# Kernel tuning notes

Hardware: AMD Instinct MI355X
Metric: run time of the kernel (lower is better)

## Reference

```python
import jax, jax.numpy as jnp
import numpy as np

DIM = 96
NHEAD = 8
HEAD_DIM = DIM // NHEAD  # 12
N, L, S = 1, 262144, 262144  # 64^3 flattened 3D volume tokens
EPS_LA = 1e-6
EPS_LN = 1e-5


def layer_norm(x, w, b):
    mu = jnp.mean(x, axis=-1, keepdims=True)
    var = jnp.mean((x - mu) ** 2, axis=-1, keepdims=True)
    return (x - mu) * jax.lax.rsqrt(var + EPS_LN) * w + b


def setup_inputs() -> dict:
    key = jax.random.key(0)
    ks = jax.random.split(key, 24)
    std = 0.02
    def w(k, shape):
        return jax.random.normal(k, shape, dtype=jnp.float32) * std
    inp = {
        "mr_seg_feat_flatten": jax.random.normal(ks[0], (N, L, DIM), dtype=jnp.float32),
        "ct2mr_attention_flatten": jax.random.normal(ks[1], (N, L, DIM), dtype=jnp.float32),
        "warp_ctfeat": jax.random.normal(ks[2], (N, S, DIM), dtype=jnp.float32),
        # CrossmodalSemanticsCalibration params (torch Linear weights: [out, in])
        "w_qkv": w(ks[3], (DIM, DIM)),
        "w_qkv2": w(ks[4], (DIM, DIM)),
        "ln1_w": jnp.ones((DIM,), jnp.float32),
        "ln1_b": jnp.zeros((DIM,), jnp.float32),
        "ln2_w": jnp.ones((2 * DIM,), jnp.float32),
        "ln2_b": jnp.zeros((2 * DIM,), jnp.float32),
        "mlp_fc1_w": w(ks[5], (2 * DIM, 2 * DIM)),
        "mlp_fc1_b": jnp.zeros((2 * DIM,), jnp.float32),
        "mlp_fc2_w": w(ks[6], (DIM, 2 * DIM)),
        "mlp_fc2_b": jnp.zeros((DIM,), jnp.float32),
        # StructureAttention(96, 8) params
        "sa_wq": w(ks[7], (DIM, DIM)),
        "sa_wk": w(ks[8], (DIM, DIM)),
        "sa_wv": w(ks[9], (DIM, DIM)),
        "sa_merge": w(ks[10], (DIM, DIM)),
        "sa_mlp_w1": w(ks[11], (2 * DIM, 2 * DIM)),
        "sa_mlp_w2": w(ks[12], (DIM, 2 * DIM)),
        "sa_ln1_w": jnp.ones((DIM,), jnp.float32),
        "sa_ln1_b": jnp.zeros((DIM,), jnp.float32),
        "sa_ln2_w": jnp.ones((DIM,), jnp.float32),
        "sa_ln2_b": jnp.zeros((DIM,), jnp.float32),
    }
    return inp


def _forward(mr_seg_feat_flatten, ct2mr_attention_flatten, warp_ctfeat,
             w_qkv, w_qkv2, ln1_w, ln1_b, ln2_w, ln2_b,
             mlp_fc1_w, mlp_fc1_b, mlp_fc2_w, mlp_fc2_b,
             sa_wq, sa_wk, sa_wv, sa_merge, sa_mlp_w1, sa_mlp_w2,
             sa_ln1_w, sa_ln1_b, sa_ln2_w, sa_ln2_b):
    # CrossmodalSemanticsCalibration.forward (ct2mr_attention_flatten is unused, as in torch)
    x0 = layer_norm(mr_seg_feat_flatten, ln1_w, ln1_b)
    shortcut = x0 @ w_qkv.T                        # [N, L, C]
    y = shortcut @ w_qkv2.T                        # [N, L, C]

    # StructureAttention(y, warp_ctfeat) with kernelized LinearAttention
    n, l, c = y.shape
    s = warp_ctfeat.shape[1]
    q = (y @ sa_wq.T).reshape(n, l, NHEAD, HEAD_DIM)
    k = (warp_ctfeat @ sa_wk.T).reshape(n, s, NHEAD, HEAD_DIM)
    v = (warp_ctfeat @ sa_wv.T).reshape(n, s, NHEAD, HEAD_DIM)
    Q = jax.nn.elu(q) + 1.0
    K = jax.nn.elu(k) + 1.0
    KV = jnp.einsum('nshd,nshv->nhdv', K, v / s)   # [N, H, d, d]
    Z = 1.0 / (jnp.einsum('nlhd,nhd->nlh', Q, K.sum(axis=1)) + EPS_LA)
    msg = jnp.einsum('nlhd,nhdv,nlh->nlhv', Q, KV, Z) * s
    msg = msg.reshape(n, l, c) @ sa_merge.T
    msg = layer_norm(msg, sa_ln1_w, sa_ln1_b)
    h = jnp.concatenate([y, msg], axis=-1) @ sa_mlp_w1.T
    h = jax.nn.relu(h) @ sa_mlp_w2.T
    h = layer_norm(h, sa_ln2_w, sa_ln2_b)
    x = y + h                                      # StructureAttention output

    # fuse with shortcut, final Mlp (GELU, exact erf as torch default)
    x = jnp.concatenate([x, shortcut], axis=-1)    # [N, L, 2C]
    x = layer_norm(x, ln2_w, ln2_b)
    x = jax.nn.gelu(x @ mlp_fc1_w.T + mlp_fc1_b, approximate=False)
    x = x @ mlp_fc2_w.T + mlp_fc2_b
    return x                                       # [N, L, C]


def reference(mr_seg_feat_flatten, ct2mr_attention_flatten, warp_ctfeat,
              w_qkv, w_qkv2, ln1_w, ln1_b, ln2_w, ln2_b,
              mlp_fc1_w, mlp_fc1_b, mlp_fc2_w, mlp_fc2_b,
              sa_wq, sa_wk, sa_wv, sa_merge, sa_mlp_w1, sa_mlp_w2,
              sa_ln1_w, sa_ln1_b, sa_ln2_w, sa_ln2_b):
    return _forward(mr_seg_feat_flatten, ct2mr_attention_flatten, warp_ctfeat,
                    w_qkv, w_qkv2, ln1_w, ln1_b, ln2_w, ln2_b,
                    mlp_fc1_w, mlp_fc1_b, mlp_fc2_w, mlp_fc2_b,
                    sa_wq, sa_wk, sa_wv, sa_merge, sa_mlp_w1, sa_mlp_w2,
                    sa_ln1_w, sa_ln1_b, sa_ln2_w, sa_ln2_b)
```

## Files before the change

### kernel.cpp

```cpp
#include <hip/hip_runtime.h>
#include <hip/hip_bf16.h>


typedef __attribute__((ext_vector_type(8))) short short8;
typedef __attribute__((ext_vector_type(4))) float f32x4;
typedef __attribute__((ext_vector_type(4))) unsigned int uint4v;

#define WS_FLAG 0
#define WS_PKV  512
#define WS_PSV  (WS_PKV + 16*9216*4)
#define WS_PSE  (WS_PSV + 16*96*4)
#define WS_KSUM (WS_PSE + 16*96*4)
#define WS_KSTOT (WS_KSUM + 96*4)
#define WS_CM   (WS_KSTOT + 64)
#define WS_BDT  (WS_CM + 768*4)
#define WS_WB   (WS_BDT + 9216*2)
#define WS_VEC  (WS_WB + 165888*2)

#define OQKV   0
#define OQKV2  9216
#define OWQ    18432
#define OWK    27648
#define OWV    36864
#define OMERGE 46080
#define OW1    55296
#define OW2    92160
#define OFC1   110592
#define OFC2   147456
#define VLN1W 0
#define VLN1B 96
#define VLN2W 192
#define VLN2B 384
#define VFC1B 576
#define VFC2B 768
#define VSA1W 864
#define VSA1B 960
#define VSA2W 1056
#define VSA2B 1152

struct InPtrs { const void* p[23]; };

__device__ inline float b2f(unsigned short x) {
  union { unsigned u; float f; } c; c.u = ((unsigned)x) << 16; return c.f;
}
__device__ inline unsigned short f2b(float f) {
  __hip_bfloat16 h = __float2bfloat16(f);
  return *(unsigned short*)&h;
}
__device__ inline uint2 pack4bf(float v0, float v1, float v2, float v3) {
  uint2 r;
  r.x = (unsigned)f2b(v0) | ((unsigned)f2b(v1) << 16);
  r.y = (unsigned)f2b(v2) | ((unsigned)f2b(v3) << 16);
  return r;
}

__global__ void probe_k(const void* in0, unsigned* flag) {
  int tid = threadIdx.x;
  const unsigned short* u = (const unsigned short*)in0;
  int cnt = 0;
  for (int j = 0; j < 8; ++j) {
    unsigned short v = u[(tid * 8 + j) * 2];
    unsigned e = (v >> 7) & 0xFF;
    if ((e >= 110 && e <= 141) || ((v & 0x7FFF) == 0)) cnt++;
  }
  for (int o = 32; o; o >>= 1) cnt += __shfl_down(cnt, o);
  if (tid == 0) *flag = (cnt > 256) ? 1u : 0u;
}

template<int ISBF>
__launch_bounds__(256)
__global__ void prep_k(InPtrs ip, char* ws) {
  if (((const unsigned*)ws)[0] != (unsigned)ISBF) return;
  const int wsrc[10] = {3,4,13,14,15,16,17,18,9,11};
  const int wdst[11] = {0,9216,18432,27648,36864,46080,55296,92160,110592,147456,165888};
  const int vsrc[10] = {5,6,7,8,10,12,19,20,21,22};
  const int vdst[11] = {0,96,192,384,576,768,864,960,1056,1152,1248};
  unsigned short* wb = (unsigned short*)(ws + WS_WB);
  float* vec = (float*)(ws + WS_VEC);
  float* zr = (float*)(ws + WS_PKV);
  const int TOT = 165888 + 1248 + 150528;
  for (int e = blockIdx.x * 256 + threadIdx.x; e < TOT; e += gridDim.x * 256) {
    if (e < 165888) {
      int w = 0;
      while (w < 9 && e >= wdst[w + 1]) ++w;
      int loc = e - wdst[w];
      if (ISBF) wb[e] = ((const unsigned short*)ip.p[wsrc[w]])[loc];
      else      wb[e] = f2b(((const float*)ip.p[wsrc[w]])[loc]);
    } else if (e < 165888 + 1248) {
      int e2 = e - 165888;
      int w = 0;
      while (w < 9 && e2 >= vdst[w + 1]) ++w;
      int loc = e2 - vdst[w];
      vec[e2] = ISBF ? b2f(((const unsigned short*)ip.p[vsrc[w]])[loc])
                     : ((const float*)ip.p[vsrc[w]])[loc];
    } else {
      zr[e - 165888 - 1248] = 0.0f;
    }
  }
}

template<int NB, int NCF, int KSTEPS>
__device__ inline void domm(const unsigned short* A, int apitch,
                            const unsigned short* B, int bpitch, int cf0,
                            int lane, f32x4 (&acc)[NB][NCF]) {
  int lr = lane & 15, lg = lane >> 4;
#pragma unroll
  for (int ks = 0; ks < KSTEPS; ++ks) {
    int k0 = ks * 32 + lg * 8;
    short8 bf[NCF];
#pragma unroll
    for (int cf = 0; cf < NCF; ++cf)
      bf[cf] = *(const short8*)(B + ((cf0 + cf) * 16 + lr) * bpitch + k0);
    short8 af[NB];
#pragma unroll
    for (int b = 0; b < NB; ++b)
      af[b] = *(const short8*)(A + (b * 16 + lr) * apitch + k0);
#pragma unroll
    for (int cf = 0; cf < NCF; ++cf)
#pragma unroll
      for (int b = 0; b < NB; ++b)
        acc[b][cf] = __builtin_amdgcn_mfma_f32_16x16x32_bf16(af[b], bf[cf], acc[b][cf], 0, 0, 0);
  }
}

template<int NB, int NCF>
__device__ inline void writeFrags(unsigned short* dst, int pitch, int cf0,
                                  int lane, f32x4 (&acc)[NB][NCF]) {
  int lr = lane & 15, lg = lane >> 4;
#pragma unroll
  for (int b = 0; b < NB; ++b)
#pragma unroll
    for (int cf = 0; cf < NCF; ++cf)
#pragma unroll
      for (int r = 0; r < 4; ++r) {
        float v = acc[b][cf][r];
        float v1 = __shfl_xor(v, 1);
        float v2 = __shfl_xor(v, 2);
        float v3 = __shfl_xor(v, 3);
        if ((lane & 3) == 0) {
          int row = b * 16 + lg * 4 + r;
          int col = (cf0 + cf) * 16 + lr;
          *(uint2*)(dst + row * pitch + col) = pack4bf(v, v1, v2, v3);
        }
      }
}

template<int NB, int NCF>
__device__ inline void zacc(f32x4 (&acc)[NB][NCF]) {
#pragma unroll
  for (int b = 0; b < NB; ++b)
#pragma unroll
    for (int cf = 0; cf < NCF; ++cf)
      acc[b][cf] = (f32x4){0.f, 0.f, 0.f, 0.f};
}

template<int ISBF>
__launch_bounds__(256)
__global__ void kA(const void* ct_, char* ws) {
  if (((const unsigned*)ws)[0] != (unsigned)ISBF) return;
  __shared__ unsigned short sCT[64][104];
  __shared__ unsigned short sEK[96][72];
  __shared__ unsigned short sVT[96][72];
  const unsigned short* Wb = (const unsigned short*)(ws + WS_WB);
  float* pKV = (float*)(ws + WS_PKV);
  int tid = threadIdx.x, lane = tid & 63, wid = tid >> 6;
  int lr = lane & 15, lg = lane >> 4;

  f32x4 kvacc[2][6];
  zacc<2, 6>(kvacc);
  float accEk = 0.f, accV = 0.f;

  for (int t = blockIdx.x; t < 4096; t += gridDim.x) {
    if (ISBF) {
      const uint4v* src = (const uint4v*)((const unsigned short*)ct_ + (size_t)t * 6144);
#pragma unroll
      for (int i = 0; i < 3; ++i) {
        int ch = tid * 3 + i;
        int r = ch / 12, c = (ch % 12) * 8;
        *(uint4v*)&sCT[r][c] = src[ch];
      }
    } else {
      const float4* src = (const float4*)((const float*)ct_ + (size_t)t * 6144);
#pragma unroll
      for (int i = 0; i < 6; ++i) {
        int ch = tid * 6 + i;
        int r = ch / 24, c = (ch % 24) * 4;
        float4 v = src[ch];
        *(uint2*)&sCT[r][c] = pack4bf(v.x, v.y, v.z, v.w);
      }
    }
    __syncthreads();

    const unsigned short* Wp = Wb + ((wid < 2) ? OWK : OWV);
    int cf0 = (wid & 1) * 3;
    f32x4 pacc[4][3];
    zacc<4, 3>(pacc);
    domm<4, 3, 3>(&sCT[0][0], 104, Wp, 96, cf0, lane, pacc);
    if (wid < 2) {
#pragma unroll
      for (int b = 0; b < 4; ++b)
#pragma unroll
        for (int cf = 0; cf < 3; ++cf)
#pragma unroll
          for (int r = 0; r < 4; ++r) {
            float v = pacc[b][cf][r];
            pacc[b][cf][r] = v > 0.f ? v : expm1f(v);
          }
    }
    {
      unsigned short* dstT = (wid < 2) ? &sEK[0][0] : &sVT[0][0];
#pragma unroll
      for (int b = 0; b < 4; ++b)
#pragma unroll
        for (int cf = 0; cf < 3; ++cf) {
          int col = (cf0 + cf) * 16 + lr;
          int t0 = b * 16 + lg * 4;
          *(uint2*)(dstT + col * 72 + t0) =
              pack4bf(pacc[b][cf][0], pacc[b][cf][1], pacc[b][cf][2], pacc[b][cf][3]);
        }
    }
    __syncthreads();

    if (wid < 3) {
#pragma unroll
      for (int ks = 0; ks < 2; ++ks) {
        int k0 = ks * 32 + lg * 8;
        short8 a[2];
#pragma unroll
        for (int bb = 0; bb < 2; ++bb)
          a[bb] = *(const short8*)&sEK[(wid * 2 + bb) * 16 + lr][k0];
#pragma unroll
        for (int cf = 0; cf < 6; ++cf) {
          short8 vb = *(const short8*)&sVT[cf * 16 + lr][k0];
#pragma unroll
          for (int bb = 0; bb < 2; ++bb)
            kvacc[bb][cf] = __builtin_amdgcn_mfma_f32_16x16x32_bf16(a[bb], vb, kvacc[bb][cf], 0, 0, 0);
        }
      }
    }
    if (tid < 96) {
#pragma unroll
      for (int j = 0; j < 8; ++j) {
        short8 e = *(const short8*)&sEK[tid][j * 8];
        short8 v = *(const short8*)&sVT[tid][j * 8];
#pragma unroll
        for (int qq = 0; qq < 8; ++qq) {
          accEk += b2f((unsigned short)e[qq]);
          accV  += b2f((unsigned short)v[qq]);
        }
      }
    }
    __syncthreads();
  }

  int slice = blockIdx.x & 15;
  if (tid < 96) {
    atomicAdd((float*)(ws + WS_PSE) + slice * 96 + tid, accEk);
    atomicAdd((float*)(ws + WS_PSV) + slice * 96 + tid, accV);
  }
  if (wid < 3) {
#pragma unroll
    for (int bb = 0; bb < 2; ++bb)
#pragma unroll
      for (int cf = 0; cf < 6; ++cf)
#pragma unroll
        for (int r = 0; r < 4; ++r) {
          int hd = (wid * 2 + bb) * 16 + lg * 4 + r;
          int hv = cf * 16 + lr;
          if (hd / 12 == hv / 12)
            atomicAdd(&pKV[slice * 9216 + hd * 96 + hv], kvacc[bb][cf][r]);
        }
  }
}

template<int ISBF>
__launch_bounds__(256)
__global__ void kFin(const void* merge_, char* ws) {
  if (((const unsigned*)ws)[0] != (unsigned)ISBF) return;
  __shared__ float Ks[96], sV[96], KV[8][12][12], csk[96];
  int tid = threadIdx.x;
  const float* pSE = (const float*)(ws + WS_PSE);
  const float* pSV = (const float*)(ws + WS_PSV);
  const float* pKV = (const float*)(ws + WS_PKV);
  if (tid < 96) {
    float a = 0.f, b = 0.f;
    for (int s = 0; s < 16; ++s) { a += pSE[s * 96 + tid]; b += pSV[s * 96 + tid]; }
    Ks[tid] = 262144.0f + a;
    sV[tid] = b;
    ((float*)(ws + WS_KSUM))[tid] = Ks[tid];
  }
  __syncthreads();
  if (tid < 8) {
    float s = 0.f;
    for (int d = 0; d < 12; ++d) s += Ks[tid * 12 + d];
    ((float*)(ws + WS_KSTOT))[tid] = s;
  }
  for (int e = tid; e < 1152; e += 256) {
    int h = e / 144, r = e % 144, d = r / 12, v = r % 12;
    int hd = h * 12 + d, hv = h * 12 + v;
    float s = sV[hv];
    for (int sl = 0; sl < 16; ++sl) s += pKV[sl * 9216 + hd * 96 + hv];
    KV[h][d][v] = s * (1.0f / 262144.0f);
  }
  unsigned short* bdt = (unsigned short*)(ws + WS_BDT);
  for (int e = tid; e < 9216; e += 256) bdt[e] = 0;
  __syncthreads();
  for (int e = tid; e < 1152; e += 256) {
    int h = e / 144, r = e % 144, d = r / 12, v = r % 12;
    bdt[(h * 12 + v) * 96 + (h * 12 + d)] = f2b(KV[h][d][v]);
  }
  if (tid < 96) {
    int h = tid / 12, v = tid % 12;
    float s = 0.f;
    for (int d = 0; d < 12; ++d) s += KV[h][d][v];
    csk[tid] = s;
  }
  __syncthreads();
  for (int e = tid; e < 768; e += 256) {
    int h = e / 96, c = e % 96;
    float s = 0.f;
    for (int v = 0; v < 12; ++v) {
      float mg = ISBF ? b2f(((const unsigned short*)merge_)[c * 96 + h * 12 + v])
                      : ((const float*)merge_)[c * 96 + h * 12 + v];
      s += csk[h * 12 + v] * mg;
    }
    ((float*)(ws + WS_CM))[e] = s;
  }
}

template<int ISBF>
__launch_bounds__(256, 3)
__global__ void kB(const void* mr_, void* out_, char* ws) {
  if (((const unsigned*)ws)[0] != (unsigned)ISBF) return;
  __shared__ unsigned short sA[64][200];
  __shared__ unsigned short sY[64][96];
  __shared__ float sZs[64][8];
  const unsigned short* Wb = (const unsigned short*)(ws + WS_WB);
  const float* vec  = (const float*)(ws + WS_VEC);
  const float* Ksum = (const float*)(ws + WS_KSUM);
  const float* KsTot = (const float*)(ws + WS_KSTOT);
  const float* CM = (const float*)(ws + WS_CM);
  const unsigned short* BDT = (const unsigned short*)(ws + WS_BDT);
  int tid = threadIdx.x, lane = tid & 63, wid = tid >> 6;
  int lr = lane & 15, lg = lane >> 4;
  int w16 = wid * 16;
  int row = tid >> 2, c0 = (tid & 3) * 24;
  int tok0 = blockIdx.x * 64;

  short8 sstash[3];

  if (ISBF) {
    const uint4v* src = (const uint4v*)((const unsigned short*)mr_ + (size_t)tok0 * 96);
#pragma unroll
    for (int i = 0; i < 3; ++i) {
      int ch = tid * 3 + i;
      int r = ch / 12, c = (ch % 12) * 8;
      *(uint4v*)&sA[r][c] = src[ch];
    }
  } else {
    const float4* src = (const float4*)((const float*)mr_ + (size_t)tok0 * 96);
#pragma unroll
    for (int i = 0; i < 6; ++i) {
      int ch = tid * 6 + i;
      int r = ch / 24, c = (ch % 24) * 4;
      float4 v = src[ch];
      *(uint2*)&sA[r][c] = pack4bf(v.x, v.y, v.z, v.w);
    }
  }
  __syncthreads();

  {
    float vals[24];
    float s = 0.f;
#pragma unroll
    for (int i = 0; i < 3; ++i) {
      short8 v = *(const short8*)&sA[row][c0 + i * 8];
#pragma unroll
      for (int j = 0; j < 8; ++j) {
        float x = b2f((unsigned short)v[j]);
        vals[i * 8 + j] = x; s += x;
      }
    }
    s += __shfl_xor(s, 1); s += __shfl_xor(s, 2);
    float mean = s * (1.f / 96.f);
    float s2 = 0.f;
#pragma unroll
    for (int j = 0; j < 24; ++j) { float d = vals[j] - mean; s2 += d * d; }
    s2 += __shfl_xor(s2, 1); s2 += __shfl_xor(s2, 2);
    float rs = rsqrtf(s2 * (1.f / 96.f) + 1e-5f);
#pragma unroll
    for (int i = 0; i < 3; ++i) {
      short8 o;
#pragma unroll
      for (int j = 0; j < 8; ++j) {
        int c = c0 + i * 8 + j;
        o[j] = (short)f2b((vals[i * 8 + j] - mean) * rs * vec[VLN1W + c] + vec[VLN1B + c]);
      }
      *(short8*)&sA[row][c0 + i * 8] = o;
    }
  }
  __syncthreads();

  f32x4 a6[1][6];
  f32x4 a12[1][12];

  zacc<1, 6>(a6);
  domm<1, 6, 3>(&sA[w16][0], 200, Wb + OQKV, 96, 0, lane, a6);
  writeFrags<1, 6>(&sA[w16][96], 200, 0, lane, a6);
  __syncthreads();

#pragma unroll
  for (int i = 0; i < 3; ++i)
    sstash[i] = *(const short8*)&sA[row][96 + c0 + i * 8];
  zacc<1, 6>(a6);
  domm<1, 6, 3>(&sA[w16][96], 200, Wb + OQKV2, 96, 0, lane, a6);
  writeFrags<1, 6>(&sY[w16][0], 96, 0, lane, a6);
  __syncthreads();

  zacc<1, 6>(a6);
  domm<1, 6, 3>(&sY[w16][0], 96, Wb + OWQ, 96, 0, lane, a6);
#pragma unroll
  for (int cf = 0; cf < 6; ++cf)
#pragma unroll
    for (int r = 0; r < 4; ++r) {
      float v = a6[0][cf][r];
      a6[0][cf][r] = v > 0.f ? v : expm1f(v);
    }
  writeFrags<1, 6>(&sA[w16][0], 200, 0, lane, a6);
  __syncthreads();

#pragma unroll
  for (int i = 0; i < 2; ++i) {
    int task = tid + 256 * i;
    int zr = task >> 3, h = task & 7;
    float den = KsTot[h];
#pragma unroll
    for (int d = 0; d < 12; ++d)
      den += b2f(sA[zr][h * 12 + d]) * Ksum[h * 12 + d];
    sZs[zr][h] = 262144.0f / (den + 1e-6f);
  }
  __syncthreads();

  zacc<1, 6>(a6);
  domm<1, 6, 3>(&sA[w16][0], 200, BDT, 96, 0, lane, a6);
#pragma unroll
  for (int cf = 0; cf < 6; ++cf) {
    int col = cf * 16 + lr;
    int h = col / 12;
#pragma unroll
    for (int r = 0; r < 4; ++r) {
      int rw = w16 + lg * 4 + r;
      a6[0][cf][r] *= sZs[rw][h];
    }
  }
  writeFrags<1, 6>(&sA[w16][96], 200, 0, lane, a6);
  __syncthreads();

  zacc<1, 6>(a6);
  domm<1, 6, 3>(&sA[w16][96], 200, Wb + OMERGE, 96, 0, lane, a6);
  writeFrags<1, 6>(&sA[w16][0], 200, 0, lane, a6);
  __syncthreads();

  {
    float vals[24];
#pragma unroll
    for (int j = 0; j < 24; ++j) vals[j] = 0.f;
#pragma unroll
    for (int h = 0; h < 8; ++h) {
      float zh = sZs[row][h];
      const float* cmr = CM + h * 96 + c0;
#pragma unroll
      for (int j = 0; j < 24; j += 4) {
        float4 c4 = *(const float4*)(cmr + j);
        vals[j] += zh * c4.x; vals[j + 1] += zh * c4.y;
        vals[j + 2] += zh * c4.z; vals[j + 3] += zh * c4.w;
      }
    }
    float s = 0.f;
#pragma unroll
    for (int i = 0; i < 3; ++i) {
      short8 v = *(const short8*)&sA[row][c0 + i * 8];
#pragma unroll
      for (int j = 0; j < 8; ++j) {
        float x = vals[i * 8 + j] + b2f((unsigned short)v[j]);
        vals[i * 8 + j] = x; s += x;
      }
    }
    s += __shfl_xor(s, 1); s += __shfl_xor(s, 2);
    float mean = s * (1.f / 96.f);
    float s2 = 0.f;
#pragma unroll
    for (int j = 0; j < 24; ++j) { float d = vals[j] - mean; s2 += d * d; }
    s2 += __shfl_xor(s2, 1); s2 += __shfl_xor(s2, 2);
    float rs = rsqrtf(s2 * (1.f / 96.f) + 1e-5f);
#pragma unroll
    for (int i = 0; i < 3; ++i) {
      short8 o;
#pragma unroll
      for (int j = 0; j < 8; ++j) {
        int c = c0 + i * 8 + j;
        o[j] = (short)f2b((vals[i * 8 + j] - mean) * rs * vec[VSA1W + c] + vec[VSA1B + c]);
      }
      *(short8*)&sA[row][96 + c0 + i * 8] = o;
    }
  }
  __syncthreads();

  zacc<1, 12>(a12);
  domm<1, 12, 3>(&sY[w16][0], 96, Wb + OW1, 192, 0, lane, a12);
  domm<1, 12, 3>(&sA[w16][96], 200, Wb + OW1 + 96, 192, 0, lane, a12);
#pragma unroll
  for (int cf = 0; cf < 12; ++cf)
#pragma unroll
    for (int r = 0; r < 4; ++r)
      a12[0][cf][r] = fmaxf(a12[0][cf][r], 0.f);
  __syncthreads();
  writeFrags<1, 12>(&sA[w16][0], 200, 0, lane, a12);
  __syncthreads();

  zacc<1, 6>(a6);
  domm<1, 6, 6>(&sA[w16][0], 200, Wb + OW2, 192, 0, lane, a6);
  __syncthreads();
  writeFrags<1, 6>(&sA[w16][0], 200, 0, lane, a6);
  __syncthreads();

  {
    float vals[24];
    float s = 0.f;
#pragma unroll
    for (int i = 0; i < 3; ++i) {
      short8 v = *(const short8*)&sA[row][c0 + i * 8];
#pragma unroll
      for (int j = 0; j < 8; ++j) {
        float x = b2f((unsigned short)v[j]);
        vals[i * 8 + j] = x; s += x;
      }
    }
    s += __shfl_xor(s, 1); s += __shfl_xor(s, 2);
    float mh = s * (1.f / 96.f);
    float s2 = 0.f;
#pragma unroll
    for (int j = 0; j < 24; ++j) { float d = vals[j] - mh; s2 += d * d; }
    s2 += __shfl_xor(s2, 1); s2 += __shfl_xor(s2, 2);
    float rh = rsqrtf(s2 * (1.f / 96.f) + 1e-5f);
    float sx = 0.f;
#pragma unroll
    for (int j = 0; j < 24; ++j) {
      int c = c0 + j;
      float x = b2f(sY[row][c]) + (vals[j] - mh) * rh * vec[VSA2W + c] + vec[VSA2B + c];
      vals[j] = x; sx += x;
    }
#pragma unroll
    for (int i = 0; i < 3; ++i)
#pragma unroll
      for (int j = 0; j < 8; ++j)
        sx += b2f((unsigned short)sstash[i][j]);
    sx += __shfl_xor(sx, 1); sx += __shfl_xor(sx, 2);
    float m2 = sx * (1.f / 192.f);
    float sx2 = 0.f;
#pragma unroll
    for (int j = 0; j < 24; ++j) { float d = vals[j] - m2; sx2 += d * d; }
#pragma unroll
    for (int i = 0; i < 3; ++i)
#pragma unroll
      for (int j = 0; j < 8; ++j) {
        float d = b2f((unsigned short)sstash[i][j]) - m2; sx2 += d * d;
      }
    sx2 += __shfl_xor(sx2, 1); sx2 += __shfl_xor(sx2, 2);
    float r2 = rsqrtf(sx2 * (1.f / 192.f) + 1e-5f);
#pragma unroll
    for (int i = 0; i < 3; ++i) {
      short8 oa, ob;
#pragma unroll
      for (int j = 0; j < 8; ++j) {
        int idx = i * 8 + j, c = c0 + idx;
        oa[j] = (short)f2b((vals[idx] - m2) * r2 * vec[VLN2W + c] + vec[VLN2B + c]);
        float sv = b2f((unsigned short)sstash[i][j]);
        ob[j] = (short)f2b((sv - m2) * r2 * vec[VLN2W + 96 + c] + vec[VLN2B + 96 + c]);
      }
      *(short8*)&sA[row][c0 + i * 8] = oa;
      *(short8*)&sA[row][96 + c0 + i * 8] = ob;
    }
  }
  __syncthreads();

  zacc<1, 12>(a12);
  domm<1, 12, 6>(&sA[w16][0], 200, Wb + OFC1, 192, 0, lane, a12);
#pragma unroll
  for (int cf = 0; cf < 12; ++cf) {
    float bb = vec[VFC1B + cf * 16 + lr];
#pragma unroll
    for (int r = 0; r < 4; ++r) {
      float x = a12[0][cf][r] + bb;
      a12[0][cf][r] = 0.5f * x * (1.0f + erff(x * 0.70710678118f));
    }
  }
  __syncthreads();
  writeFrags<1, 12>(&sA[w16][0], 200, 0, lane, a12);
  __syncthreads();

  zacc<1, 6>(a6);
  domm<1, 6, 6>(&sA[w16][0], 200, Wb + OFC2, 192, 0, lane, a6);
#pragma unroll
  for (int cf = 0; cf < 6; ++cf) {
    int col = cf * 16 + lr;
    float bias = vec[VFC2B + col];
#pragma unroll
    for (int r = 0; r < 4; ++r) {
      float v = a6[0][cf][r] + bias;
      float v1 = __shfl_xor(v, 1);
      float v2 = __shfl_xor(v, 2);
      float v3 = __shfl_xor(v, 3);
      if ((lane & 3) == 0) {
        size_t token = (size_t)tok0 + w16 + lg * 4 + r;
        size_t off = token * 96 + col;
        if (ISBF) {
          *(uint2*)((unsigned short*)out_ + off) = pack4bf(v, v1, v2, v3);
        } else {
          float4 f; f.x = v; f.y = v1; f.z = v2; f.w = v3;
          *(float4*)((float*)out_ + off) = f;
        }
      }
    }
  }
}

extern "C" void kernel_launch(void* const* d_in, const int* in_sizes, int n_in,
                              void* d_out, int out_size, void* d_ws, size_t ws_size,
                              hipStream_t stream) {
  (void)in_sizes; (void)n_in; (void)out_size; (void)ws_size;
  char* ws = (char*)d_ws;
  probe_k<<<1, 64, 0, stream>>>(d_in[0], (unsigned*)ws);
  InPtrs ip;
  for (int i = 0; i < 23; ++i) ip.p[i] = d_in[i];
  prep_k<0><<<512, 256, 0, stream>>>(ip, ws);
  prep_k<1><<<512, 256, 0, stream>>>(ip, ws);
  kA<0><<<1024, 256, 0, stream>>>(d_in[2], ws);
  kA<1><<<1024, 256, 0, stream>>>(d_in[2], ws);
  kFin<0><<<1, 256, 0, stream>>>(d_in[16], ws);
  kFin<1><<<1, 256, 0, stream>>>(d_in[16], ws);
  kB<0><<<4096, 256, 0, stream>>>(d_in[0], d_out, ws);
  kB<1><<<4096, 256, 0, stream>>>(d_in[0], d_out, ws);
}
```

Baseline: 766.2 us.

## Stage weight tiles in shared memory for kB matmuls instead of global loads

Each MFMA matmul in the fused token kernel now first copies a 96x96 weight chunk into a padded LDS buffer cooperatively, then reads B fragments from LDS. Previously every wave read the weight fragments directly from global memory (cache). Larger matmuls are split into 96x96 chunks with extra barriers, sY is padded, and the launch-bounds occupancy hint is dropped. This adds roughly 20KB LDS per block and many syncthreads, which may reduce occupancy and serialize staging with compute.

```diff
diff --git a/kernel.cpp b/kernel.cpp
--- a/kernel.cpp
+++ b/kernel.cpp
@@ -123,26 +123,61 @@
   }
 }
 
-template<int NB, int NCF>
-__device__ inline void writeFrags(unsigned short* dst, int pitch, int cf0,
-                                  int lane, f32x4 (&acc)[NB][NCF]) {
+template<int NCF, int CFOFF>
+__device__ inline void dommL(const unsigned short* A, int apitch, int akoff,
+                             const unsigned short (&sB)[96][104],
+                             int lane, f32x4 (&acc)[12]) {
   int lr = lane & 15, lg = lane >> 4;
 #pragma unroll
-  for (int b = 0; b < NB; ++b)
+  for (int ks = 0; ks < 3; ++ks) {
+    int k0 = ks * 32 + lg * 8;
+    short8 bf[NCF];
 #pragma unroll
     for (int cf = 0; cf < NCF; ++cf)
-#pragma unroll
-      for (int r = 0; r < 4; ++r) {
-        float v = acc[b][cf][r];
-        float v1 = __shfl_xor(v, 1);
-        float v2 = __shfl_xor(v, 2);
-        float v3 = __shfl_xor(v, 3);
-        if ((lane & 3) == 0) {
-          int row = b * 16 + lg * 4 + r;
-          int col = (cf0 + cf) * 16 + lr;
-          *(uint2*)(dst + row * pitch + col) = pack4bf(v, v1, v2, v3);
-        }
-      }
+      bf[cf] = *(const short8*)&sB[cf * 16 + lr][k0];
+    short8 af = *(const short8*)(A + lr * apitch + akoff + k0);
+#pragma unroll
+    for (int cf = 0; cf < NCF; ++cf)
+      acc[CFOFF + cf] = __builtin_amdgcn_mfma_f32_16x16x32_bf16(af, bf[cf], acc[CFOFF + cf], 0, 0, 0);
+  }
+}
+
+__device__ inline void stageB(const unsigned short* src, int bpitch, int tid,
+                              unsigned short (&sB)[96][104]) {
+#pragma unroll
+  for (int i = 0; i < 5; ++i) {
+    int ch = tid + 256 * i;
+    if (ch < 1152) {
+      int row = ch / 12, col = (ch % 12) * 8;
+      *(uint4v*)&sB[row][col] = *(const uint4v*)(src + row * bpitch + col);
+    }
+  }
+}
+
+template<int NCF>
+__device__ inline void writeF(unsigned short* dst, int pitch, int lane,
+                              f32x4 (&acc)[12]) {
+  int lr = lane & 15, lg = lane >> 4;
+#pragma unroll
+  for (int cf = 0; cf < NCF; ++cf)
+#pragma unroll
+    for (int r = 0; r < 4; ++r) {
+      float v = acc[cf][r];
+      float v1 = __shfl_xor(v, 1);
+      float v2 = __shfl_xor(v, 2);
+      float v3 = __shfl_xor(v, 3);
+      if ((lane & 3) == 0) {
+        int row = lg * 4 + r;
+        int col = cf * 16 + lr;
+        *(uint2*)(dst + row * pitch + col) = pack4bf(v, v1, v2, v3);
+      }
+    }
+}
+
+__device__ inline void zacc12(f32x4 (&acc)[12], int n) {
+#pragma unroll
+  for (int i = 0; i < 12; ++i)
+    if (i < n) acc[i] = (f32x4){0.f, 0.f, 0.f, 0.f};
 }
 
 template<int NB, int NCF>
@@ -329,11 +364,12 @@
 }
 
 template<int ISBF>
-__launch_bounds__(256, 3)
+__launch_bounds__(256)
 __global__ void kB(const void* mr_, void* out_, char* ws) {
   if (((const unsigned*)ws)[0] != (unsigned)ISBF) return;
   __shared__ unsigned short sA[64][200];
-  __shared__ unsigned short sY[64][96];
+  __shared__ unsigned short sY[64][104];
+  __shared__ unsigned short sB[96][104];
   __shared__ float sZs[64][8];
   const unsigned short* Wb = (const unsigned short*)(ws + WS_WB);
   const float* vec  = (const float*)(ws + WS_VEC);
@@ -398,51 +434,60 @@
       }
       *(short8*)&sA[row][c0 + i * 8] = o;
     }
-  }
-  __syncthreads();
-
-  f32x4 a6[1][6];
-  f32x4 a12[1][12];
-
-  zacc<1, 6>(a6);
-  domm<1, 6, 3>(&sA[w16][0], 200, Wb + OQKV, 96, 0, lane, a6);
-  writeFrags<1, 6>(&sA[w16][96], 200, 0, lane, a6);
+    stageB(Wb + OQKV, 96, tid, sB);
+  }
+  __syncthreads();
+
+  f32x4 acc[12];
+
+  zacc12(acc, 6);
+  dommL<6, 0>(&sA[w16][0], 200, 0, sB, lane, acc);
+  writeF<6>(&sA[w16][96], 200, lane, acc);
   __syncthreads();
 
 #pragma unroll
   for (int i = 0; i < 3; ++i)
     sstash[i] = *(const short8*)&sA[row][96 + c0 + i * 8];
-  zacc<1, 6>(a6);
-  domm<1, 6, 3>(&sA[w16][96], 200, Wb + OQKV2, 96, 0, lane, a6);
-  writeFrags<1, 6>(&sY[w16][0], 96, 0, lane, a6);
-  __syncthreads();
-
-  zacc<1, 6>(a6);
-  domm<1, 6, 3>(&sY[w16][0], 96, Wb + OWQ, 96, 0, lane, a6);
+  stageB(Wb + OQKV2, 96, tid, sB);
+  __syncthreads();
+
+  zacc12(acc, 6);
+  dommL<6, 0>(&sA[w16][96], 200, 0, sB, lane, acc);
+  writeF<6>(&sY[w16][0], 104, lane, acc);
+  __syncthreads();
+
+  stageB(Wb + OWQ, 96, tid, sB);
+  __syncthreads();
+
+  zacc12(acc, 6);
+  dommL<6, 0>(&sY[w16][0], 104, 0, sB, lane, acc);
 #pragma unroll
   for (int cf = 0; cf < 6; ++cf)
 #pragma unroll
     for (int r = 0; r < 4; ++r) {
-      float v = a6[0][cf][r];
-      a6[0][cf][r] = v > 0.f ? v : expm1f(v);
-    }
-  writeFrags<1, 6>(&sA[w16][0], 200, 0, lane, a6);
-  __syncthreads();
-
-#pragma unroll
-  for (int i = 0; i < 2; ++i) {
-    int task = tid + 256 * i;
-    int zr = task >> 3, h = task & 7;
-    float den = KsTot[h];
-#pragma unroll
-    for (int d = 0; d < 12; ++d)
-      den += b2f(sA[zr][h * 12 + d]) * Ksum[h * 12 + d];
-    sZs[zr][h] = 262144.0f / (den + 1e-6f);
-  }
-  __syncthreads();
-
-  zacc<1, 6>(a6);
-  domm<1, 6, 3>(&sA[w16][0], 200, BDT, 96, 0, lane, a6);
+      float v = acc[cf][r];
+      acc[cf][r] = v > 0.f ? v : expm1f(v);
+    }
+  writeF<6>(&sA[w16][0], 200, lane, acc);
+  __syncthreads();
+
+  {
+    stageB(BDT, 96, tid, sB);
+#pragma unroll
+    for (int i = 0; i < 2; ++i) {
+      int task = tid + 256 * i;
+      int zr = task >> 3, h = task & 7;
+      float den = KsTot[h];
+#pragma unroll
+      for (int d = 0; d < 12; ++d)
+        den += b2f(sA[zr][h * 12 + d]) * Ksum[h * 12 + d];
+      sZs[zr][h] = 262144.0f / (den + 1e-6f);
+    }
+  }
+  __syncthreads();
+
+  zacc12(acc, 6);
+  dommL<6, 0>(&sA[w16][0], 200, 0, sB, lane, acc);
 #pragma unroll
   for (int cf = 0; cf < 6; ++cf) {
     int col = cf * 16 + lr;
@@ -450,15 +495,18 @@
 #pragma unroll
     for (int r = 0; r < 4; ++r) {
       int rw = w16 + lg * 4 + r;
-      a6[0][cf][r] *= sZs[rw][h];
-    }
-  }
-  writeFrags<1, 6>(&sA[w16][96], 200, 0, lane, a6);
-  __syncthreads();
-
-  zacc<1, 6>(a6);
-  domm<1, 6, 3>(&sA[w16][96], 200, Wb + OMERGE, 96, 0, lane, a6);
-  writeFrags<1, 6>(&sA[w16][0], 200, 0, lane, a6);
+      acc[cf][r] *= sZs[rw][h];
+    }
+  }
+  writeF<6>(&sA[w16][96], 200, lane, acc);
+  __syncthreads();
+
+  stageB(Wb + OMERGE, 96, tid, sB);
+  __syncthreads();
+
+  zacc12(acc, 6);
+  dommL<6, 0>(&sA[w16][96], 200, 0, sB, lane, acc);
+  writeF<6>(&sA[w16][0], 200, lane, acc);
   __syncthreads();
 
   {
@@ -503,25 +551,43 @@
       }
       *(short8*)&sA[row][96 + c0 + i * 8] = o;
     }
-  }
-  __syncthreads();
-
-  zacc<1, 12>(a12);
-  domm<1, 12, 3>(&sY[w16][0], 96, Wb + OW1, 192, 0, lane, a12);
-  domm<1, 12, 3>(&sA[w16][96], 200, Wb + OW1 + 96, 192, 0, lane, a12);
+    stageB(Wb + OW1, 192, tid, sB);
+  }
+  __syncthreads();
+
+  zacc12(acc, 12);
+  dommL<6, 0>(&sY[w16][0], 104, 0, sB, lane, acc);
+  __syncthreads();
+  stageB(Wb + OW1 + 96, 192, tid, sB);
+  __syncthreads();
+  dommL<6, 0>(&sA[w16][96], 200, 0, sB, lane, acc);
+  __syncthreads();
+  stageB(Wb + OW1 + 96 * 192, 192, tid, sB);
+  __syncthreads();
+  dommL<6, 6>(&sY[w16][0], 104, 0, sB, lane, acc);
+  __syncthreads();
+  stageB(Wb + OW1 + 96 * 192 + 96, 192, tid, sB);
+  __syncthreads();
+  dommL<6, 6>(&sA[w16][96], 200, 0, sB, lane, acc);
 #pragma unroll
   for (int cf = 0; cf < 12; ++cf)
 #pragma unroll
     for (int r = 0; r < 4; ++r)
-      a12[0][cf][r] = fmaxf(a12[0][cf][r], 0.f);
-  __syncthreads();
-  writeFrags<1, 12>(&sA[w16][0], 200, 0, lane, a12);
-  __syncthreads();
-
-  zacc<1, 6>(a6);
-  domm<1, 6, 6>(&sA[w16][0], 200, Wb + OW2, 192, 0, lane, a6);
-  __syncthreads();
-  writeFrags<1, 6>(&sA[w16][0], 200, 0, lane, a6);
+      acc[cf][r] = fmaxf(acc[cf][r], 0.f);
+  __syncthreads();
+  writeF<12>(&sA[w16][0], 200, lane, acc);
+  __syncthreads();
+
+  stageB(Wb + OW2, 192, tid, sB);
+  __syncthreads();
+  zacc12(acc, 6);
+  dommL<6, 0>(&sA[w16][0], 200, 0, sB, lane, acc);
+  __syncthreads();
+  stageB(Wb + OW2 + 96, 192, tid, sB);
+  __syncthreads();
+  dommL<6, 0>(&sA[w16][0], 200, 96, sB, lane, acc);
+  __syncthreads();
+  writeF<6>(&sA[w16][0], 200, lane, acc);
   __syncthreads();
 
   {
@@ -581,33 +647,52 @@
       *(short8*)&sA[row][c0 + i * 8] = oa;
       *(short8*)&sA[row][96 + c0 + i * 8] = ob;
     }
-  }
-  __syncthreads();
-
-  zacc<1, 12>(a12);
-  domm<1, 12, 6>(&sA[w16][0], 200, Wb + OFC1, 192, 0, lane, a12);
+    stageB(Wb + OFC1, 192, tid, sB);
+  }
+  __syncthreads();
+
+  zacc12(acc, 12);
+  dommL<6, 0>(&sA[w16][0], 200, 0, sB, lane, acc);
+  __syncthreads();
+  stageB(Wb + OFC1 + 96, 192, tid, sB);
+  __syncthreads();
+  dommL<6, 0>(&sA[w16][96], 200, 0, sB, lane, acc);
+  __syncthreads();
+  stageB(Wb + OFC1 + 96 * 192, 192, tid, sB);
+  __syncthreads();
+  dommL<6, 6>(&sA[w16][0], 200, 0, sB, lane, acc);
+  __syncthreads();
+  stageB(Wb + OFC1 + 96 * 192 + 96, 192, tid, sB);
+  __syncthreads();
+  dommL<6, 6>(&sA[w16][96], 200, 0, sB, lane, acc);
 #pragma unroll
   for (int cf = 0; cf < 12; ++cf) {
     float bb = vec[VFC1B + cf * 16 + lr];
 #pragma unroll
     for (int r = 0; r < 4; ++r) {
-      float x = a12[0][cf][r] + bb;
-      a12[0][cf][r] = 0.5f * x * (1.0f + erff(x * 0.70710678118f));
-    }
-  }
-  __syncthreads();
-  writeFrags<1, 12>(&sA[w16][0], 200, 0, lane, a12);
-  __syncthreads();
-
-  zacc<1, 6>(a6);
-  domm<1, 6, 6>(&sA[w16][0], 200, Wb + OFC2, 192, 0, lane, a6);
+      float x = acc[cf][r] + bb;
+      acc[cf][r] = 0.5f * x * (1.0f + erff(x * 0.70710678118f));
+    }
+  }
+  __syncthreads();
+  writeF<12>(&sA[w16][0], 200, lane, acc);
+  __syncthreads();
+
+  stageB(Wb + OFC2, 192, tid, sB);
+  __syncthreads();
+  zacc12(acc, 6);
+  dommL<6, 0>(&sA[w16][0], 200, 0, sB, lane, acc);
+  __syncthreads();
+  stageB(Wb + OFC2 + 96, 192, tid, sB);
+  __syncthreads();
+  dommL<6, 0>(&sA[w16][96], 200, 0, sB, lane, acc);
 #pragma unroll
   for (int cf = 0; cf < 6; ++cf) {
     int col = cf * 16 + lr;
     float bias = vec[VFC2B + col];
 #pragma unroll
     for (int r = 0; r < 4; ++r) {
-      float v = a6[0][cf][r] + bias;
+      float v = acc[cf][r] + bias;
       float v1 = __shfl_xor(v, 1);
       float v2 = __shfl_xor(v, 2);
       float v3 = __shfl_xor(v, 3);
```

After: 933.4 us. 21.8% more time.
